# Kernel optimization log

Hardware: AMD Instinct MI355X
Metric: run time of the kernel (lower is better)

The kernel has to match this reference:

```python
import jax, jax.numpy as jnp
import numpy as np

NUM_HEADS = 16
ROPE_BASE = 10000.0
NEG_INF = float('-inf')


def _rotate_half_interleaved(x):
    # x: [..., d]; interleaved rotation: (-x2, x1) pairs
    x1 = x[..., ::2]
    x2 = x[..., 1::2]
    return jnp.stack((-x2, x1), axis=-1).reshape(x.shape)


def _rope_tables(seq_len, head_dim, dtype):
    inv_freq = 1.0 / (ROPE_BASE ** (jnp.arange(0, head_dim, 2, dtype=jnp.float32) / head_dim))
    pos = jnp.arange(seq_len, dtype=jnp.float32)
    freqs = pos[:, None] * inv_freq[None, :]          # [S, d/2]
    emb = jnp.concatenate((freqs, freqs), axis=-1)    # [S, d]  (HF-style concat, as in source)
    return jnp.cos(emb).astype(dtype), jnp.sin(emb).astype(dtype)


def setup_inputs() -> dict:
    key = jax.random.key(0)
    ks = jax.random.split(key, 4)
    B, S, H = 2, 2048, 2048
    scale = 0.02
    x = jax.random.normal(ks[0], (B, S, H), dtype=jnp.float32)
    qkv_w = jax.random.normal(ks[1], (3 * H, H), dtype=jnp.float32) * scale
    qkv_b = jnp.zeros((3 * H,), dtype=jnp.float32)
    out_w = jax.random.normal(ks[2], (H, H), dtype=jnp.float32) * scale
    out_b = jnp.zeros((H,), dtype=jnp.float32)
    attention_mask = jnp.ones((B, S), dtype=jnp.int32)
    return {"x": x, "attention_mask": attention_mask, "qkv_w": qkv_w,
            "qkv_b": qkv_b, "out_w": out_w, "out_b": out_b}


def reference(x, attention_mask, qkv_w, qkv_b, out_w, out_b):
    B, S, H = x.shape
    nh = NUM_HEADS
    hd = H // nh
    scale = hd ** -0.5

    qkv = x @ qkv_w.T + qkv_b                            # [B,S,3H]
    qkv = qkv.reshape(B, S, 3, nh, hd).transpose(2, 0, 3, 1, 4)  # [3,B,nh,S,hd]
    q, k, v = qkv[0], qkv[1], qkv[2]

    cos, sin = _rope_tables(S, hd, x.dtype)              # [S,hd]
    cos = cos[None, None, :, :]
    sin = sin[None, None, :, :]
    q = q * cos + _rotate_half_interleaved(q) * sin
    k = k * cos + _rotate_half_interleaved(k) * sin

    scores = jnp.einsum('bhqd,bhkd->bhqk', q, k) * scale  # [B,nh,S,S]
    causal = jnp.triu(jnp.ones((S, S), dtype=bool), k=1)
    scores = jnp.where(causal[None, None], NEG_INF, scores)
    key_mask = (attention_mask == 0)[:, None, None, :]    # [B,1,1,S]
    scores = jnp.where(key_mask, NEG_INF, scores)

    weights = jax.nn.softmax(scores, axis=-1)
    attn = jnp.einsum('bhqk,bhkd->bhqd', weights, v)       # [B,nh,S,hd]
    attn = attn.transpose(0, 2, 1, 3).reshape(B, S, H)
    return attn @ out_w.T + out_b
```

## Files before the change

kernel.cpp:

```cpp
#include <hip/hip_runtime.h>

typedef __bf16 bf16;
typedef __bf16 bf16x2 __attribute__((ext_vector_type(2)));
typedef __bf16 bf16x4 __attribute__((ext_vector_type(4)));
typedef __bf16 bf16x8 __attribute__((ext_vector_type(8)));
typedef float f32x4 __attribute__((ext_vector_type(4)));
typedef float f32x16 __attribute__((ext_vector_type(16)));

#define MFMA_BF16(a, b, c) __builtin_amdgcn_mfma_f32_16x16x32_bf16(a, b, c, 0, 0, 0)
#define MFMA32(a, b, c)    __builtin_amdgcn_mfma_f32_32x32x16_bf16(a, b, c, 0, 0, 0)

__device__ __forceinline__ void async16(const void* g, void* l) {
    __builtin_amdgcn_global_load_lds(
        (const __attribute__((address_space(1))) void*)g,
        (__attribute__((address_space(3))) void*)l,
        16, 0, 0);
}

__device__ __forceinline__ unsigned pack2(float a, float b) {
    bf16x2 t; t[0] = (bf16)a; t[1] = (bf16)b;
    return __builtin_bit_cast(unsigned, t);
}

__device__ __forceinline__ void cvt8_body(const float* __restrict__ in,
                                          bf16* __restrict__ out, int blk) {
    int i = (blk * 256 + (int)threadIdx.x) * 8;
    float4 a = *(const float4*)(in + i);
    float4 b = *(const float4*)(in + i + 4);
    bf16x8 o;
    o[0] = (bf16)a.x; o[1] = (bf16)a.y; o[2] = (bf16)a.z; o[3] = (bf16)a.w;
    o[4] = (bf16)b.x; o[5] = (bf16)b.y; o[6] = (bf16)b.z; o[7] = (bf16)b.w;
    *(bf16x8*)(out + i) = o;
}

__global__ void prep(const float* __restrict__ x, const float* __restrict__ qkvw,
                     const float* __restrict__ outw, const int* __restrict__ am,
                     bf16* __restrict__ xb, bf16* __restrict__ wqkv, bf16* __restrict__ wout,
                     float* __restrict__ cosT, float* __restrict__ sinT,
                     float* __restrict__ mbias) {
    int blk = blockIdx.x;
    if (blk < 4096)        cvt8_body(x,    xb,   blk);
    else if (blk < 10240)  cvt8_body(qkvw, wqkv, blk - 4096);
    else if (blk < 12288)  cvt8_body(outw, wout, blk - 10240);
    else {
        int i = (blk - 12288) * 256 + threadIdx.x;
        int s = i >> 7, d = i & 127, fi = d & 63;
        float inv = exp2f(-(float)fi * (13.287712379549449f / 64.0f));
        float ang = (float)s * inv;
        cosT[i] = cosf(ang);
        sinT[i] = sinf(ang);
        if (i < 2 * 2048) mbias[i] = (am[i] == 0) ? -1.4427e30f : 0.0f;
    }
}

template <int EPI>
__global__ void __launch_bounds__(256, 2)
gemm_bt(const bf16* __restrict__ A, const bf16* __restrict__ Bt,
        const float* __restrict__ bias, float* __restrict__ Cf,
        bf16* __restrict__ qb, bf16* __restrict__ kb, bf16* __restrict__ vtb,
        const float* __restrict__ cosT, const float* __restrict__ sinT,
        int M, int N, int K) {
    __shared__ __align__(16) bf16 sA[128 * 64];
    __shared__ __align__(16) bf16 sB[128 * 64];
    const int tid  = threadIdx.x;
    const int lane = tid & 63;
    const int quad = lane >> 4, l15 = lane & 15;
    const int wid = tid >> 6, wm = wid >> 1, wn = wid & 1;
    const int bm = blockIdx.x, bn = blockIdx.y;

    f32x4 acc[4][4];
#pragma unroll
    for (int i = 0; i < 4; i++)
#pragma unroll
        for (int j = 0; j < 4; j++)
#pragma unroll
            for (int c = 0; c < 4; c++) acc[i][j][c] = 0.0f;

    const int r0 = tid >> 3, x0 = tid & 7;
    const int g0 = x0 ^ (r0 & 7);
    const bf16* pa = A  + (size_t)(bm * 128 + r0) * K + g0 * 8;
    const bf16* pb = Bt + (size_t)(bn * 128 + r0) * K + g0 * 8;
    bf16* la = sA + tid * 8;
    bf16* lb = sB + tid * 8;
    const size_t gstep = (size_t)32 * K;

    for (int k0 = 0; k0 < K; k0 += 64) {
#pragma unroll
        for (int i = 0; i < 4; i++) {
            async16(pa + i * gstep, la + i * 2048);
            async16(pb + i * gstep, lb + i * 2048);
        }
        pa += 64; pb += 64;
        __syncthreads();
#pragma unroll
        for (int ks = 0; ks < 2; ks++) {
            bf16x8 af[4], bfr[4];
#pragma unroll
            for (int i = 0; i < 4; i++) {
                int r = wm * 64 + i * 16 + l15;
                int x = (ks * 4 + quad) ^ (r & 7);
                af[i] = *(const bf16x8*)(sA + r * 64 + x * 8);
            }
#pragma unroll
            for (int i = 0; i < 4; i++) {
                int r = wn * 64 + i * 16 + l15;
                int x = (ks * 4 + quad) ^ (r & 7);
                bfr[i] = *(const bf16x8*)(sB + r * 64 + x * 8);
            }
#pragma unroll
            for (int mi = 0; mi < 4; mi++)
#pragma unroll
                for (int ni = 0; ni < 4; ni++)
                    acc[mi][ni] = MFMA_BF16(af[mi], bfr[ni], acc[mi][ni]);
        }
        __syncthreads();
    }

    if (EPI == 0) {
#pragma unroll
        for (int mi = 0; mi < 4; mi++)
#pragma unroll
            for (int ni = 0; ni < 4; ni++) {
                int row0 = bm * 128 + wm * 64 + mi * 16 + quad * 4;
                int col  = bn * 128 + wn * 64 + ni * 16 + l15;
                float bv = bias[col];
#pragma unroll
                for (int r = 0; r < 4; r++)
                    Cf[(size_t)(row0 + r) * N + col] = acc[mi][ni][r] + bv;
            }
    } else {
#pragma unroll
        for (int mi = 0; mi < 4; mi++)
#pragma unroll
            for (int ni = 0; ni < 4; ni++) {
                int col   = bn * 128 + wn * 64 + ni * 16 + l15;
                int which = col >> 11;
                int hcol  = col & 2047;
                int h = hcol >> 7, d = hcol & 127;
                float bv = bias[col];
#pragma unroll
                for (int r = 0; r < 4; r++) {
                    int row = bm * 128 + wm * 64 + mi * 16 + quad * 4 + r;
                    int b = row >> 11, s = row & 2047;
                    float v  = acc[mi][ni][r] + bv;
                    float vp = __shfl_xor(v, 1, 64);
                    float ov = v;
                    if (which < 2) {
                        float c  = cosT[(s << 7) + d];
                        float sn = sinT[(s << 7) + d];
                        ov = v * c + ((d & 1) ? vp : -vp) * sn;
                    }
                    if (which == 0) ov *= 0.12751743f;
                    size_t bh = (size_t)(b * 16 + h);
                    if (which == 0)      qb[(bh * 2048 + s) * 128 + d] = (bf16)ov;
                    else if (which == 1) kb[(bh * 2048 + s) * 128 + d] = (bf16)ov;
                    else                 vtb[(bh * 128 + d) * 2048 + s] = (bf16)ov;
                }
            }
    }
}

__global__ void __launch_bounds__(256, 2)
fattn(const bf16* __restrict__ Q, const bf16* __restrict__ Kg,
      const bf16* __restrict__ Vt, const float* __restrict__ mbias,
      bf16* __restrict__ O, float* __restrict__ Opart, float* __restrict__ mlpart) {
    __shared__ __align__(16) bf16 sK[2][64 * 128];
    __shared__ __align__(16) bf16 sV[2][128 * 64];
    const int tid = threadIdx.x, lane = tid & 63, w = tid >> 6;
    const int l31 = lane & 31, half = lane >> 5;
    const int id = (int)blockIdx.x;
    const int bh = id & 31, v = id >> 5;
    const int p = v >> 1, role = v & 1;
    const int qa = 15 - p;
    const int n1 = role ? (15 - 2 * p) : 17;

    const bf16* Qb  = Q  + (size_t)bh * 2048 * 128;
    const bf16* Kbh = Kg + (size_t)bh * 2048 * 128;
    const bf16* Vbh = Vt + (size_t)bh * 128 * 2048;
    const int b = bh >> 4, hh = bh & 15;
    const float* mbb = mbias + b * 2048;

    const int swk = (l31 & 15) ^ (l31 >> 4);
    const int swv = (l31 & 7) ^ ((l31 >> 3) & 3);
    const int rk = tid >> 4, xk = tid & 15, gkb = xk ^ rk;
    const int rv = tid >> 3, xv = tid & 7;
    const int gv = xv ^ (rv & 7) ^ ((rv >> 3) & 3);

    auto KT = [&](int t) { return role ? (t < n1 ? 17 + t : t - n1) : t; };

    int qt = qa;
    int myq  = qt * 128 + w * 32 + l31;
    int qmin = qt * 128 + w * 32;

    bf16x8 qf[8];
#pragma unroll
    for (int kq = 0; kq < 8; kq++)
        qf[kq] = *(const bf16x8*)(Qb + (size_t)myq * 128 + kq * 16 + half * 8);

    f32x16 oacc[4];
#pragma unroll
    for (int dt = 0; dt < 4; dt++)
#pragma unroll
        for (int c = 0; c < 16; c++) oacc[dt][c] = 0.0f;
    float m_s = -3e38f, l_s = 0.0f;

    {
        int kb0 = KT(0) * 64;
#pragma unroll
        for (int i = 0; i < 4; i++) {
            async16(Kbh + (size_t)(kb0 + rk + i * 16) * 128 + (gkb ^ (i & 1)) * 8,
                    &sK[0][(i * 256 + tid) * 8]);
            async16(Vbh + (size_t)(rv + i * 32) * 2048 + kb0 + gv * 8,
                    &sV[0][(i * 256 + tid) * 8]);
        }
    }
    __syncthreads();

    for (int t = 0; t < 17; t++) {
        if (role && t == n1) {
            float lf = l_s + __shfl_xor(l_s, 32, 64);
            size_t slot = (size_t)(bh * 8 + (qa - 8)) * 2 + 1;
            float* op = Opart + slot * 16384 + (size_t)(w * 32 + l31) * 128;
#pragma unroll
            for (int dt = 0; dt < 4; dt++)
#pragma unroll
                for (int g = 0; g < 4; g++) {
                    float4 o4 = make_float4(oacc[dt][g * 4 + 0], oacc[dt][g * 4 + 1],
                                            oacc[dt][g * 4 + 2], oacc[dt][g * 4 + 3]);
                    *(float4*)(op + dt * 32 + 8 * g + 4 * half) = o4;
                }
            if (half == 0) {
                float* mp = mlpart + (slot * 128 + (w * 32 + l31)) * 2;
                mp[0] = m_s; mp[1] = lf;
            }
#pragma unroll
            for (int dt = 0; dt < 4; dt++)
#pragma unroll
                for (int c = 0; c < 16; c++) oacc[dt][c] = 0.0f;
            m_s = -3e38f; l_s = 0.0f;
            qt = p;
            myq  = qt * 128 + w * 32 + l31;
            qmin = qt * 128 + w * 32;
#pragma unroll
            for (int kq = 0; kq < 8; kq++)
                qf[kq] = *(const bf16x8*)(Qb + (size_t)myq * 128 + kq * 16 + half * 8);
        }

        const int kb0 = KT(t) * 64;
        const int buf = t & 1;
        if (t + 1 < 17) {
            const int nb0 = KT(t + 1) * 64;
#pragma unroll
            for (int i = 0; i < 4; i++) {
                async16(Kbh + (size_t)(nb0 + rk + i * 16) * 128 + (gkb ^ (i & 1)) * 8,
                        &sK[buf ^ 1][(i * 256 + tid) * 8]);
                async16(Vbh + (size_t)(rv + i * 32) * 2048 + nb0 + gv * 8,
                        &sV[buf ^ 1][(i * 256 + tid) * 8]);
            }
        }
        const bf16* sKb = sK[buf];
        const bf16* sVb = sV[buf];

        f32x16 sacc[2];
#pragma unroll
        for (int tt = 0; tt < 2; tt++)
#pragma unroll
            for (int c = 0; c < 16; c++) sacc[tt][c] = 0.0f;
#pragma unroll
        for (int kq = 0; kq < 8; kq++) {
#pragma unroll
            for (int tt = 0; tt < 2; tt++) {
                int row = tt * 32 + l31;
                int x = (kq * 2 + half) ^ swk;
                bf16x8 kf = *(const bf16x8*)(sKb + row * 128 + x * 8);
                sacc[tt] = MFMA32(kf, qf[kq], sacc[tt]);
            }
        }

        float mx = -3e38f;
        if (kb0 + 63 < qmin) {
#pragma unroll
            for (int tt = 0; tt < 2; tt++)
#pragma unroll
                for (int g = 0; g < 4; g++) {
                    float4 mb4 = *(const float4*)(mbb + kb0 + tt * 32 + 8 * g + 4 * half);
#pragma unroll
                    for (int r2 = 0; r2 < 4; r2++) {
                        float vv = sacc[tt][g * 4 + r2] + ((const float*)&mb4)[r2];
                        sacc[tt][g * 4 + r2] = vv;
                        mx = fmaxf(mx, vv);
                    }
                }
        } else {
#pragma unroll
            for (int tt = 0; tt < 2; tt++)
#pragma unroll
                for (int g = 0; g < 4; g++) {
                    float4 mb4 = *(const float4*)(mbb + kb0 + tt * 32 + 8 * g + 4 * half);
#pragma unroll
                    for (int r2 = 0; r2 < 4; r2++) {
                        int sk = kb0 + tt * 32 + 8 * g + 4 * half + r2;
                        float vv = sacc[tt][g * 4 + r2] + ((const float*)&mb4)[r2];
                        vv = (sk > myq) ? -1e30f : vv;
                        sacc[tt][g * 4 + r2] = vv;
                        mx = fmaxf(mx, vv);
                    }
                }
        }

        mx = fmaxf(mx, __shfl_xor(mx, 32, 64));
        float mnew  = fmaxf(m_s, mx);
        float alpha = exp2f(m_s - mnew);
        float rs = 0.0f;
#pragma unroll
        for (int tt = 0; tt < 2; tt++)
#pragma unroll
            for (int c = 0; c < 16; c++) {
                float pe = exp2f(sacc[tt][c] - mnew);
                sacc[tt][c] = pe;
                rs += pe;
            }
        l_s = l_s * alpha + rs;
        m_s = mnew;
#pragma unroll
        for (int dt = 0; dt < 4; dt++) oacc[dt] *= alpha;

#pragma unroll
        for (int tt = 0; tt < 2; tt++) {
            unsigned w8[8];
#pragma unroll
            for (int i = 0; i < 8; i++)
                w8[i] = pack2(sacc[tt][2 * i], sacc[tt][2 * i + 1]);
#pragma unroll
            for (int s2 = 0; s2 < 2; s2++) {
                const int bse = 4 * s2;
                unsigned a0 = half ? w8[bse]     : w8[bse + 2];
                unsigned a1 = half ? w8[bse + 1] : w8[bse + 3];
                unsigned z0 = (unsigned)__shfl_xor((int)a0, 32, 64);
                unsigned z1 = (unsigned)__shfl_xor((int)a1, 32, 64);
                union { unsigned u[4]; bf16x8 vv; } pu;
                pu.u[0] = half ? z0 : w8[bse];
                pu.u[1] = half ? z1 : w8[bse + 1];
                pu.u[2] = half ? w8[bse + 2] : z0;
                pu.u[3] = half ? w8[bse + 3] : z1;
                bf16x8 pf = pu.vv;
                const int c = (tt * 2 + s2) * 2 + half;
#pragma unroll
                for (int dt = 0; dt < 4; dt++) {
                    int row = dt * 32 + l31;
                    int x = c ^ swv;
                    bf16x8 vf = *(const bf16x8*)(sVb + row * 64 + x * 8);
                    oacc[dt] = MFMA32(vf, pf, oacc[dt]);
                }
            }
        }
        __syncthreads();
    }

    float lf = l_s + __shfl_xor(l_s, 32, 64);
    if (role == 0) {
        size_t slot = (size_t)(bh * 8 + (qa - 8)) * 2 + 0;
        float* op = Opart + slot * 16384 + (size_t)(w * 32 + l31) * 128;
#pragma unroll
        for (int dt = 0; dt < 4; dt++)
#pragma unroll
            for (int g = 0; g < 4; g++) {
                float4 o4 = make_float4(oacc[dt][g * 4 + 0], oacc[dt][g * 4 + 1],
                                        oacc[dt][g * 4 + 2], oacc[dt][g * 4 + 3]);
                *(float4*)(op + dt * 32 + 8 * g + 4 * half) = o4;
            }
        if (half == 0) {
            float* mp = mlpart + (slot * 128 + (w * 32 + l31)) * 2;
            mp[0] = m_s; mp[1] = lf;
        }
    } else {
        float inv = 1.0f / lf;
        size_t base = ((size_t)(b * 2048 + myq)) * 2048 + hh * 128;
#pragma unroll
        for (int dt = 0; dt < 4; dt++)
#pragma unroll
            for (int g = 0; g < 4; g++) {
                bf16x4 o4;
#pragma unroll
                for (int r2 = 0; r2 < 4; r2++) o4[r2] = (bf16)(oacc[dt][g * 4 + r2] * inv);
                *(bf16x4*)(O + base + dt * 32 + 8 * g + 4 * half) = o4;
            }
    }
}

__global__ void combine(const float* __restrict__ Opart, const float* __restrict__ mlpart,
                        bf16* __restrict__ attn) {
    int i = blockIdx.x * 256 + threadIdx.x;
    int dq = (i & 31) * 4;
    int row = i >> 5;
    int qloc = row & 127, ba = row >> 7;
    int ai = ba & 7, bh = ba >> 3;
    const float* mlA = mlpart + ((size_t)(ba * 2 + 0) * 128 + qloc) * 2;
    const float* mlB = mlpart + ((size_t)(ba * 2 + 1) * 128 + qloc) * 2;
    float mA = mlA[0], lA = mlA[1], mB = mlB[0], lB = mlB[1];
    float m = fmaxf(mA, mB);
    float wA = exp2f(mA - m), wB = exp2f(mB - m);
    float inv = 1.0f / (wA * lA + wB * lB);
    float4 oA = *(const float4*)(Opart + (size_t)(ba * 2 + 0) * 16384 + qloc * 128 + dq);
    float4 oB = *(const float4*)(Opart + (size_t)(ba * 2 + 1) * 16384 + qloc * 128 + dq);
    int q = (8 + ai) * 128 + qloc;
    int b = bh >> 4, hh = bh & 15;
    bf16x4 o4;
    o4[0] = (bf16)((wA * oA.x + wB * oB.x) * inv);
    o4[1] = (bf16)((wA * oA.y + wB * oB.y) * inv);
    o4[2] = (bf16)((wA * oA.z + wB * oB.z) * inv);
    o4[3] = (bf16)((wA * oA.w + wB * oB.w) * inv);
    *(bf16x4*)(attn + ((size_t)(b * 2048 + q)) * 2048 + hh * 128 + dq) = o4;
}

extern "C" void kernel_launch(void* const* d_in, const int* in_sizes, int n_in,
                              void* d_out, int out_size, void* d_ws, size_t ws_size,
                              hipStream_t stream) {
    const float* x     = (const float*)d_in[0];
    const int*   am    = (const int*)d_in[1];
    const float* qkvw  = (const float*)d_in[2];
    const float* qkvb  = (const float*)d_in[3];
    const float* outw  = (const float*)d_in[4];
    const float* outb  = (const float*)d_in[5];
    float* out = (float*)d_out;

    char* ws = (char*)d_ws;
    bf16*  xb    = (bf16*)(ws);
    bf16*  wqkv  = (bf16*)(ws + (16ull << 20));
    bf16*  wout  = (bf16*)(ws + (40ull << 20));
    bf16*  qb    = (bf16*)(ws + (48ull << 20));
    bf16*  kb    = (bf16*)(ws + (64ull << 20));
    bf16*  vtb   = (bf16*)(ws + (80ull << 20));
    bf16*  attn  = (bf16*)(ws + (96ull << 20));
    float* cosT  = (float*)(ws + (112ull << 20));
    float* sinT  = (float*)(ws + (113ull << 20));
    float* mbias = (float*)(ws + (114ull << 20));
    float* Opart  = (float*)(ws);
    float* mlpart = (float*)(ws + (32ull << 20));

    prep<<<13312, 256, 0, stream>>>(x, qkvw, outw, am, xb, wqkv, wout, cosT, sinT, mbias);

    gemm_bt<1><<<dim3(32, 48), 256, 0, stream>>>(
        xb, wqkv, qkvb, nullptr, qb, kb, vtb, cosT, sinT, 4096, 6144, 2048);

    fattn<<<dim3(512), 256, 0, stream>>>(qb, kb, vtb, mbias, attn, Opart, mlpart);

    combine<<<4096, 256, 0, stream>>>(Opart, mlpart, attn);

    gemm_bt<0><<<dim3(32, 16), 256, 0, stream>>>(
        attn, wout, outb, out, nullptr, nullptr, nullptr, nullptr, nullptr,
        4096, 2048, 2048);
}
```

Measured before the change: 385.6 us.

## Switch GEMMs to 32x32 MFMA and fuse split-KV combine into attention via tickets

The GEMM inner loop now uses 32x32x16 bf16 MFMA tiles (2x2 per wave) instead of 16x16x32 (4x4), with an adjusted LDS swizzle. This halves the LDS fragment reads per MFMA and should cut LDS bandwidth pressure. Separately, the standalone combine kernel is removed: each split attention block bumps an atomic ticket after writing its partial, and the second finisher merges both partials into the output. This drops a launch and a pass over the partials, at the cost of fences, an extra block-wide barrier and a serialized merge tail in some blocks.

```diff
diff --git a/kernel.cpp b/kernel.cpp
--- a/kernel.cpp
+++ b/kernel.cpp
@@ -4,11 +4,9 @@
 typedef __bf16 bf16x2 __attribute__((ext_vector_type(2)));
 typedef __bf16 bf16x4 __attribute__((ext_vector_type(4)));
 typedef __bf16 bf16x8 __attribute__((ext_vector_type(8)));
-typedef float f32x4 __attribute__((ext_vector_type(4)));
 typedef float f32x16 __attribute__((ext_vector_type(16)));
 
-#define MFMA_BF16(a, b, c) __builtin_amdgcn_mfma_f32_16x16x32_bf16(a, b, c, 0, 0, 0)
-#define MFMA32(a, b, c)    __builtin_amdgcn_mfma_f32_32x32x16_bf16(a, b, c, 0, 0, 0)
+#define MFMA32(a, b, c) __builtin_amdgcn_mfma_f32_32x32x16_bf16(a, b, c, 0, 0, 0)
 
 __device__ __forceinline__ void async16(const void* g, void* l) {
     __builtin_amdgcn_global_load_lds(
@@ -37,7 +35,7 @@
                      const float* __restrict__ outw, const int* __restrict__ am,
                      bf16* __restrict__ xb, bf16* __restrict__ wqkv, bf16* __restrict__ wout,
                      float* __restrict__ cosT, float* __restrict__ sinT,
-                     float* __restrict__ mbias) {
+                     float* __restrict__ mbias, int* __restrict__ ticket) {
     int blk = blockIdx.x;
     if (blk < 4096)        cvt8_body(x,    xb,   blk);
     else if (blk < 10240)  cvt8_body(qkvw, wqkv, blk - 4096);
@@ -50,6 +48,7 @@
         cosT[i] = cosf(ang);
         sinT[i] = sinf(ang);
         if (i < 2 * 2048) mbias[i] = (am[i] == 0) ? -1.4427e30f : 0.0f;
+        if (i < 256) ticket[i] = 0;
     }
 }
 
@@ -64,25 +63,26 @@
     __shared__ __align__(16) bf16 sB[128 * 64];
     const int tid  = threadIdx.x;
     const int lane = tid & 63;
-    const int quad = lane >> 4, l15 = lane & 15;
+    const int l31 = lane & 31, half = lane >> 5;
     const int wid = tid >> 6, wm = wid >> 1, wn = wid & 1;
     const int bm = blockIdx.x, bn = blockIdx.y;
 
-    f32x4 acc[4][4];
-#pragma unroll
-    for (int i = 0; i < 4; i++)
-#pragma unroll
-        for (int j = 0; j < 4; j++)
-#pragma unroll
-            for (int c = 0; c < 4; c++) acc[i][j][c] = 0.0f;
+    f32x16 acc[2][2];
+#pragma unroll
+    for (int i = 0; i < 2; i++)
+#pragma unroll
+        for (int j = 0; j < 2; j++)
+#pragma unroll
+            for (int c = 0; c < 16; c++) acc[i][j][c] = 0.0f;
 
     const int r0 = tid >> 3, x0 = tid & 7;
-    const int g0 = x0 ^ (r0 & 7);
+    const int g0 = x0 ^ (r0 & 7) ^ ((r0 >> 3) & 3);
     const bf16* pa = A  + (size_t)(bm * 128 + r0) * K + g0 * 8;
     const bf16* pb = Bt + (size_t)(bn * 128 + r0) * K + g0 * 8;
     bf16* la = sA + tid * 8;
     bf16* lb = sB + tid * 8;
     const size_t gstep = (size_t)32 * K;
+    const int swz = (l31 & 7) ^ ((l31 >> 3) & 3);
 
     for (int k0 = 0; k0 < K; k0 += 64) {
 #pragma unroll
@@ -93,85 +93,119 @@
         pa += 64; pb += 64;
         __syncthreads();
 #pragma unroll
-        for (int ks = 0; ks < 2; ks++) {
-            bf16x8 af[4], bfr[4];
-#pragma unroll
-            for (int i = 0; i < 4; i++) {
-                int r = wm * 64 + i * 16 + l15;
-                int x = (ks * 4 + quad) ^ (r & 7);
-                af[i] = *(const bf16x8*)(sA + r * 64 + x * 8);
-            }
-#pragma unroll
-            for (int i = 0; i < 4; i++) {
-                int r = wn * 64 + i * 16 + l15;
-                int x = (ks * 4 + quad) ^ (r & 7);
-                bfr[i] = *(const bf16x8*)(sB + r * 64 + x * 8);
-            }
-#pragma unroll
-            for (int mi = 0; mi < 4; mi++)
-#pragma unroll
-                for (int ni = 0; ni < 4; ni++)
-                    acc[mi][ni] = MFMA_BF16(af[mi], bfr[ni], acc[mi][ni]);
+        for (int kc = 0; kc < 4; kc++) {
+            const int x = (kc * 2 + half) ^ swz;
+            bf16x8 af[2], bf_[2];
+#pragma unroll
+            for (int t = 0; t < 2; t++) {
+                int rA = wm * 64 + t * 32 + l31;
+                int rB = wn * 64 + t * 32 + l31;
+                af[t]  = *(const bf16x8*)(sA + rA * 64 + x * 8);
+                bf_[t] = *(const bf16x8*)(sB + rB * 64 + x * 8);
+            }
+#pragma unroll
+            for (int ti = 0; ti < 2; ti++)
+#pragma unroll
+                for (int tj = 0; tj < 2; tj++)
+                    acc[ti][tj] = MFMA32(af[ti], bf_[tj], acc[ti][tj]);
         }
         __syncthreads();
     }
 
     if (EPI == 0) {
 #pragma unroll
-        for (int mi = 0; mi < 4; mi++)
-#pragma unroll
-            for (int ni = 0; ni < 4; ni++) {
-                int row0 = bm * 128 + wm * 64 + mi * 16 + quad * 4;
-                int col  = bn * 128 + wn * 64 + ni * 16 + l15;
+        for (int ti = 0; ti < 2; ti++)
+#pragma unroll
+            for (int tj = 0; tj < 2; tj++) {
+                int col = bn * 128 + wn * 64 + tj * 32 + l31;
                 float bv = bias[col];
 #pragma unroll
-                for (int r = 0; r < 4; r++)
-                    Cf[(size_t)(row0 + r) * N + col] = acc[mi][ni][r] + bv;
+                for (int g = 0; g < 4; g++)
+#pragma unroll
+                    for (int r2 = 0; r2 < 4; r2++) {
+                        int row = bm * 128 + wm * 64 + ti * 32 + 8 * g + 4 * half + r2;
+                        Cf[(size_t)row * N + col] = acc[ti][tj][4 * g + r2] + bv;
+                    }
             }
     } else {
 #pragma unroll
-        for (int mi = 0; mi < 4; mi++)
-#pragma unroll
-            for (int ni = 0; ni < 4; ni++) {
-                int col   = bn * 128 + wn * 64 + ni * 16 + l15;
+        for (int ti = 0; ti < 2; ti++)
+#pragma unroll
+            for (int tj = 0; tj < 2; tj++) {
+                int col   = bn * 128 + wn * 64 + tj * 32 + l31;
                 int which = col >> 11;
                 int hcol  = col & 2047;
                 int h = hcol >> 7, d = hcol & 127;
                 float bv = bias[col];
 #pragma unroll
-                for (int r = 0; r < 4; r++) {
-                    int row = bm * 128 + wm * 64 + mi * 16 + quad * 4 + r;
-                    int b = row >> 11, s = row & 2047;
-                    float v  = acc[mi][ni][r] + bv;
-                    float vp = __shfl_xor(v, 1, 64);
-                    float ov = v;
-                    if (which < 2) {
-                        float c  = cosT[(s << 7) + d];
-                        float sn = sinT[(s << 7) + d];
-                        ov = v * c + ((d & 1) ? vp : -vp) * sn;
+                for (int g = 0; g < 4; g++)
+#pragma unroll
+                    for (int r2 = 0; r2 < 4; r2++) {
+                        int row = bm * 128 + wm * 64 + ti * 32 + 8 * g + 4 * half + r2;
+                        int b = row >> 11, s = row & 2047;
+                        float v  = acc[ti][tj][4 * g + r2] + bv;
+                        float vp = __shfl_xor(v, 1, 64);
+                        float ov = v;
+                        if (which < 2) {
+                            float c  = cosT[(s << 7) + d];
+                            float sn = sinT[(s << 7) + d];
+                            ov = v * c + ((d & 1) ? vp : -vp) * sn;
+                        }
+                        if (which == 0) ov *= 0.12751743f;
+                        size_t bh = (size_t)(b * 16 + h);
+                        if (which == 0)      qb[(bh * 2048 + s) * 128 + d] = (bf16)ov;
+                        else if (which == 1) kb[(bh * 2048 + s) * 128 + d] = (bf16)ov;
+                        else                 vtb[(bh * 128 + d) * 2048 + s] = (bf16)ov;
                     }
-                    if (which == 0) ov *= 0.12751743f;
-                    size_t bh = (size_t)(b * 16 + h);
-                    if (which == 0)      qb[(bh * 2048 + s) * 128 + d] = (bf16)ov;
-                    else if (which == 1) kb[(bh * 2048 + s) * 128 + d] = (bf16)ov;
-                    else                 vtb[(bh * 128 + d) * 2048 + s] = (bf16)ov;
-                }
-            }
+            }
+    }
+}
+
+__device__ __forceinline__ void merge_slot(const float* __restrict__ Opart,
+                                           const float* __restrict__ mlpart,
+                                           bf16* __restrict__ attn,
+                                           int bh, int qa, int tid) {
+    int b = bh >> 4, hh = bh & 15;
+    size_t sA = (size_t)(bh * 8 + (qa - 8)) * 2;
+    const float* oA = Opart + sA * 16384;
+    const float* oB = oA + 16384;
+#pragma unroll
+    for (int it = 0; it < 16; it++) {
+        int li = it * 256 + tid;
+        int qloc = li >> 5, dq = (li & 31) * 4;
+        const float* mlA = mlpart + (sA * 128 + qloc) * 2;
+        const float* mlB = mlpart + ((sA + 1) * 128 + qloc) * 2;
+        float mA = mlA[0], lA = mlA[1], mB = mlB[0], lB = mlB[1];
+        float m = fmaxf(mA, mB);
+        float wA = exp2f(mA - m), wB = exp2f(mB - m);
+        float inv = 1.0f / (wA * lA + wB * lB);
+        float4 a4 = *(const float4*)(oA + qloc * 128 + dq);
+        float4 b4 = *(const float4*)(oB + qloc * 128 + dq);
+        int s = qa * 128 + qloc;
+        bf16x4 o4;
+        o4[0] = (bf16)((wA * a4.x + wB * b4.x) * inv);
+        o4[1] = (bf16)((wA * a4.y + wB * b4.y) * inv);
+        o4[2] = (bf16)((wA * a4.z + wB * b4.z) * inv);
+        o4[3] = (bf16)((wA * a4.w + wB * b4.w) * inv);
+        *(bf16x4*)(attn + ((size_t)(b * 2048 + s)) * 2048 + hh * 128 + dq) = o4;
     }
 }
 
 __global__ void __launch_bounds__(256, 2)
 fattn(const bf16* __restrict__ Q, const bf16* __restrict__ Kg,
       const bf16* __restrict__ Vt, const float* __restrict__ mbias,
-      bf16* __restrict__ O, float* __restrict__ Opart, float* __restrict__ mlpart) {
+      bf16* __restrict__ O, float* __restrict__ Opart, float* __restrict__ mlpart,
+      int* __restrict__ ticket) {
     __shared__ __align__(16) bf16 sK[2][64 * 128];
     __shared__ __align__(16) bf16 sV[2][128 * 64];
+    __shared__ int sWin;
     const int tid = threadIdx.x, lane = tid & 63, w = tid >> 6;
     const int l31 = lane & 31, half = lane >> 5;
     const int id = (int)blockIdx.x;
     const int bh = id & 31, v = id >> 5;
     const int p = v >> 1, role = v & 1;
     const int qa = 15 - p;
+    const int idx = bh * 8 + (qa - 8);
     const int n1 = role ? (15 - 2 * p) : 17;
 
     const bf16* Qb  = Q  + (size_t)bh * 2048 * 128;
@@ -191,6 +225,7 @@
     int qt = qa;
     int myq  = qt * 128 + w * 32 + l31;
     int qmin = qt * 128 + w * 32;
+    bool mergeWin = false;
 
     bf16x8 qf[8];
 #pragma unroll
@@ -219,7 +254,7 @@
     for (int t = 0; t < 17; t++) {
         if (role && t == n1) {
             float lf = l_s + __shfl_xor(l_s, 32, 64);
-            size_t slot = (size_t)(bh * 8 + (qa - 8)) * 2 + 1;
+            size_t slot = (size_t)idx * 2 + 1;
             float* op = Opart + slot * 16384 + (size_t)(w * 32 + l31) * 128;
 #pragma unroll
             for (int dt = 0; dt < 4; dt++)
@@ -233,6 +268,11 @@
                 float* mp = mlpart + (slot * 128 + (w * 32 + l31)) * 2;
                 mp[0] = m_s; mp[1] = lf;
             }
+            __threadfence();
+            __syncthreads();
+            if (tid == 0) sWin = (atomicAdd(ticket + idx, 1) == 1) ? 1 : 0;
+            __syncthreads();
+            mergeWin = (sWin != 0);
 #pragma unroll
             for (int dt = 0; dt < 4; dt++)
 #pragma unroll
@@ -359,7 +399,7 @@
 
     float lf = l_s + __shfl_xor(l_s, 32, 64);
     if (role == 0) {
-        size_t slot = (size_t)(bh * 8 + (qa - 8)) * 2 + 0;
+        size_t slot = (size_t)idx * 2;
         float* op = Opart + slot * 16384 + (size_t)(w * 32 + l31) * 128;
 #pragma unroll
         for (int dt = 0; dt < 4; dt++)
@@ -373,6 +413,11 @@
             float* mp = mlpart + (slot * 128 + (w * 32 + l31)) * 2;
             mp[0] = m_s; mp[1] = lf;
         }
+        __threadfence();
+        __syncthreads();
+        if (tid == 0) sWin = (atomicAdd(ticket + idx, 1) == 1) ? 1 : 0;
+        __syncthreads();
+        mergeWin = (sWin != 0);
     } else {
         float inv = 1.0f / lf;
         size_t base = ((size_t)(b * 2048 + myq)) * 2048 + hh * 128;
@@ -386,31 +431,11 @@
                 *(bf16x4*)(O + base + dt * 32 + 8 * g + 4 * half) = o4;
             }
     }
-}
-
-__global__ void combine(const float* __restrict__ Opart, const float* __restrict__ mlpart,
-                        bf16* __restrict__ attn) {
-    int i = blockIdx.x * 256 + threadIdx.x;
-    int dq = (i & 31) * 4;
-    int row = i >> 5;
-    int qloc = row & 127, ba = row >> 7;
-    int ai = ba & 7, bh = ba >> 3;
-    const float* mlA = mlpart + ((size_t)(ba * 2 + 0) * 128 + qloc) * 2;
-    const float* mlB = mlpart + ((size_t)(ba * 2 + 1) * 128 + qloc) * 2;
-    float mA = mlA[0], lA = mlA[1], mB = mlB[0], lB = mlB[1];
-    float m = fmaxf(mA, mB);
-    float wA = exp2f(mA - m), wB = exp2f(mB - m);
-    float inv = 1.0f / (wA * lA + wB * lB);
-    float4 oA = *(const float4*)(Opart + (size_t)(ba * 2 + 0) * 16384 + qloc * 128 + dq);
-    float4 oB = *(const float4*)(Opart + (size_t)(ba * 2 + 1) * 16384 + qloc * 128 + dq);
-    int q = (8 + ai) * 128 + qloc;
-    int b = bh >> 4, hh = bh & 15;
-    bf16x4 o4;
-    o4[0] = (bf16)((wA * oA.x + wB * oB.x) * inv);
-    o4[1] = (bf16)((wA * oA.y + wB * oB.y) * inv);
-    o4[2] = (bf16)((wA * oA.z + wB * oB.z) * inv);
-    o4[3] = (bf16)((wA * oA.w + wB * oB.w) * inv);
-    *(bf16x4*)(attn + ((size_t)(b * 2048 + q)) * 2048 + hh * 128 + dq) = o4;
+
+    if (mergeWin) {
+        __threadfence();
+        merge_slot(Opart, mlpart, O, bh, qa, tid);
+    }
 }
 
 extern "C" void kernel_launch(void* const* d_in, const int* in_sizes, int n_in,
@@ -435,17 +460,17 @@
     float* cosT  = (float*)(ws + (112ull << 20));
     float* sinT  = (float*)(ws + (113ull << 20));
     float* mbias = (float*)(ws + (114ull << 20));
+    int*   tick  = (int*)(ws + (114ull << 20) + 65536);
     float* Opart  = (float*)(ws);
     float* mlpart = (float*)(ws + (32ull << 20));
 
-    prep<<<13312, 256, 0, stream>>>(x, qkvw, outw, am, xb, wqkv, wout, cosT, sinT, mbias);
+    prep<<<13312, 256, 0, stream>>>(x, qkvw, outw, am, xb, wqkv, wout,
+                                    cosT, sinT, mbias, tick);
 
     gemm_bt<1><<<dim3(32, 48), 256, 0, stream>>>(
         xb, wqkv, qkvb, nullptr, qb, kb, vtb, cosT, sinT, 4096, 6144, 2048);
 
-    fattn<<<dim3(512), 256, 0, stream>>>(qb, kb, vtb, mbias, attn, Opart, mlpart);
-
-    combine<<<4096, 256, 0, stream>>>(Opart, mlpart, attn);
+    fattn<<<dim3(512), 256, 0, stream>>>(qb, kb, vtb, mbias, attn, Opart, mlpart, tick);
 
     gemm_bt<0><<<dim3(32, 16), 256, 0, stream>>>(
         attn, wout, outb, out, nullptr, nullptr, nullptr, nullptr, nullptr,
```

Result: slower. 470.9 us (+22.1%).
